# Kernel optimization log

Hardware: AMD Instinct MI355X
Metric: run time of the kernel (lower is better)

## Reference

```python
import jax, jax.numpy as jnp
import numpy as np
from jax import lax

EPS = 1e-5
NBIT = 127.0  # 8-bit symmetric: 2^(8-1)-1

def ste_round(x):
    return x + lax.stop_gradient(jnp.round(x) - x)

def quant_act(x, rng_max):
    # symmetric fake-quant of activations with learned per-cluster range
    s = rng_max / NBIT
    xq = jnp.clip(ste_round(x / s), -NBIT, NBIT) * s
    return xq, s

def fold_bn(w, gamma, beta, mean, var):
    std = jnp.sqrt(var + EPS)
    scale = gamma / std
    w_f = w * scale[:, None, None, None]
    b_f = beta - mean * scale
    return w_f, b_f

def quant_weight(w):
    # per-output-channel symmetric quant
    s = jnp.max(jnp.abs(w), axis=(1, 2, 3), keepdims=True) / NBIT
    wq = jnp.clip(ste_round(w / s), -NBIT, NBIT) * s
    return wq, s.reshape(-1)

def conv(x, w, stride=1, groups=1, pad=0):
    return lax.conv_general_dilated(
        x, w, window_strides=(stride, stride),
        padding=((pad, pad), (pad, pad)),
        dimension_numbers=('NCHW', 'OIHW', 'NCHW'),
        feature_group_count=groups)

def setup_inputs() -> dict:
    key = jax.random.key(0)
    ks = jax.random.split(key, 24)
    B, Cin, H, W = 64, 96, 28, 28
    Cmid, Cout, NC = 576, 96, 4
    d = {}
    d['x'] = jax.random.normal(ks[0], (B, Cin, H, W), dtype=jnp.float32)
    # conv1: 1x1 expansion
    d['w1'] = jax.random.normal(ks[1], (Cmid, Cin, 1, 1), jnp.float32) * 0.1
    d['g1'] = jax.random.uniform(ks[2], (Cmid,), minval=0.5, maxval=1.5)
    d['b1'] = jax.random.normal(ks[3], (Cmid,)) * 0.1
    d['m1'] = jax.random.normal(ks[4], (Cmid,)) * 0.1
    d['v1'] = jax.random.uniform(ks[5], (Cmid,), minval=0.5, maxval=1.5)
    # conv2: 3x3 depthwise
    d['w2'] = jax.random.normal(ks[6], (Cmid, 1, 3, 3), jnp.float32) * 0.1
    d['g2'] = jax.random.uniform(ks[7], (Cmid,), minval=0.5, maxval=1.5)
    d['b2'] = jax.random.normal(ks[8], (Cmid,)) * 0.1
    d['m2'] = jax.random.normal(ks[9], (Cmid,)) * 0.1
    d['v2'] = jax.random.uniform(ks[10], (Cmid,), minval=0.5, maxval=1.5)
    # conv3: 1x1 projection
    d['w3'] = jax.random.normal(ks[11], (Cout, Cmid, 1, 1), jnp.float32) * 0.1
    d['g3'] = jax.random.uniform(ks[12], (Cout,), minval=0.5, maxval=1.5)
    d['b3'] = jax.random.normal(ks[13], (Cout,)) * 0.1
    d['m3'] = jax.random.normal(ks[14], (Cout,)) * 0.1
    d['v3'] = jax.random.uniform(ks[15], (Cout,), minval=0.5, maxval=1.5)
    # per-cluster learned activation ranges for the 4 QuantAct modules
    d['r0'] = jax.random.uniform(ks[16], (NC,), minval=2.0, maxval=8.0)
    d['r1'] = jax.random.uniform(ks[17], (NC,), minval=2.0, maxval=8.0)
    d['r2'] = jax.random.uniform(ks[18], (NC,), minval=2.0, maxval=8.0)
    d['r3'] = jax.random.uniform(ks[19], (NC,), minval=2.0, maxval=8.0)
    d['cluster'] = 2
    return d

def reference(x, w1, g1, b1, m1, v1, w2, g2, b2, m2, v2,
              w3, g3, b3, m3, v3, r0, r1, r2, r3, cluster):
    identity = x  # residual path (in==out, stride==1)
    # QuantAct -> conv1 (BN-folded, per-channel quant) -> ReLU6
    xq, s0 = quant_act(x, r0[cluster])
    w1f, bf1 = fold_bn(w1, g1, b1, m1, v1)
    w1q, ws1 = quant_weight(w1f)
    y = conv(xq, w1q) + bf1[None, :, None, None]
    y = jnp.clip(y, 0.0, 6.0)
    # QuantAct1 -> depthwise conv2 -> ReLU6
    yq, s1 = quant_act(y, r1[cluster])
    w2f, bf2 = fold_bn(w2, g2, b2, m2, v2)
    w2q, ws2 = quant_weight(w2f)
    y = conv(yq, w2q, stride=1, groups=w2.shape[0], pad=1) + bf2[None, :, None, None]
    y = jnp.clip(y, 0.0, 6.0)
    # QuantAct2 -> conv3 projection
    yq, s2 = quant_act(y, r2[cluster])
    w3f, bf3 = fold_bn(w3, g3, b3, m3, v3)
    w3q, ws3 = quant_weight(w3f)
    y = conv(yq, w3q) + bf3[None, :, None, None]
    # residual add, then int32 requant
    y = y + identity
    out, s3 = quant_act(y, r3[cluster])
    return out, s3
```

## Files before the change

kernel.cpp:

```cpp
#include <hip/hip_runtime.h>
#include <cstdint>
#include <cstddef>

typedef int   v4i __attribute__((ext_vector_type(4)));
typedef float v4f __attribute__((ext_vector_type(4)));
typedef unsigned int u32;

constexpr int B_   = 64;
constexpr int CIN  = 96;
constexpr int P_   = 784;
constexpr int CMID = 576;
constexpr int COUT = 96;
constexpr int NOUT = B_ * COUT * P_;
constexpr float NBITF = 127.0f;
constexpr float EPSF  = 1e-5f;
constexpr float MAGICF = 12582912.0f;
constexpr int   BIASI  = 0x4B400000;

constexpr int Y1S = 43;

__device__ __forceinline__ int dot3(u32 a, u32 w, int acc) {
#if __has_builtin(__builtin_amdgcn_sdot4)
    return __builtin_amdgcn_sdot4((int)a, (int)w, acc, false);
#else
    return acc + (int)(signed char)(a)        * (int)(signed char)(w)
               + (int)(signed char)(a >> 8)   * (int)(signed char)(w >> 8)
               + (int)(signed char)(a >> 16)  * (int)(signed char)(w >> 16);
#endif
}

__device__ __forceinline__ void tr4(u32 S0, u32 S1, u32 S2, u32 S3, u32 O[4]) {
    u32 u01 = __builtin_amdgcn_perm(S1, S0, 0x05010400u);
    u32 u23 = __builtin_amdgcn_perm(S3, S2, 0x05010400u);
    u32 v01 = __builtin_amdgcn_perm(S1, S0, 0x07030602u);
    u32 v23 = __builtin_amdgcn_perm(S3, S2, 0x07030602u);
    O[0] = __builtin_amdgcn_perm(u23, u01, 0x05040100u);
    O[1] = __builtin_amdgcn_perm(u23, u01, 0x07060302u);
    O[2] = __builtin_amdgcn_perm(v23, v01, 0x05040100u);
    O[3] = __builtin_amdgcn_perm(v23, v01, 0x07060302u);
}

__device__ __forceinline__ u32 pack4(u32 t0, u32 t1, u32 t2, u32 t3) {
    u32 p01 = __builtin_amdgcn_perm(t1, t0, 0x05010400u);
    u32 p23 = __builtin_amdgcn_perm(t3, t2, 0x05010400u);
    return __builtin_amdgcn_perm(p23, p01, 0x05040100u);
}

__global__ __launch_bounds__(256)
void prep_w(const float* __restrict__ w1, const float* __restrict__ g1,
            const float* __restrict__ b1, const float* __restrict__ m1,
            const float* __restrict__ v1,
            const float* __restrict__ w2, const float* __restrict__ g2,
            const float* __restrict__ b2, const float* __restrict__ m2,
            const float* __restrict__ v2,
            const float* __restrict__ w3, const float* __restrict__ g3,
            const float* __restrict__ b3, const float* __restrict__ m3,
            const float* __restrict__ v3,
            const float* __restrict__ r0, const float* __restrict__ r1,
            const float* __restrict__ r2, const int* __restrict__ cluster,
            int8_t* __restrict__ w1qp, float2* __restrict__ e1,
            v4i* __restrict__ w2pk,    float2* __restrict__ e2,
            int8_t* __restrict__ w3qp, float2* __restrict__ e3)
{
    int tid = threadIdx.x;
    int c = cluster[0];
    int lane = tid & 63, wv = tid >> 6;
    int blk = blockIdx.x * 4 + wv;

    const float *w, *g, *bb, *mm, *vv;
    int oc, K, which;
    if (blk < CMID)            { which = 0; w = w1; g = g1; bb = b1; mm = m1; vv = v1; oc = blk;            K = CIN;  }
    else if (blk < 2 * CMID)   { which = 1; w = w2; g = g2; bb = b2; mm = m2; vv = v2; oc = blk - CMID;     K = 9;    }
    else                       { which = 2; w = w3; g = g3; bb = b3; mm = m3; vv = v3; oc = blk - 2 * CMID; K = CMID; }

    float scale = g[oc] / sqrtf(vv[oc] + EPSF);

    float mx = 0.f;
    for (int k = lane; k < K; k += 64)
        mx = fmaxf(mx, fabsf(w[oc * K + k] * scale));
    #pragma unroll
    for (int off = 1; off < 64; off <<= 1)
        mx = fmaxf(mx, __shfl_xor(mx, off));

    float s = mx / NBITF;

    int myq = 0;
    for (int k = lane; k < K; k += 64) {
        float wf = w[oc * K + k] * scale;
        float q  = fminf(fmaxf(rintf(wf / s), -127.f), 127.f);
        if (which == 0)      w1qp[oc * 144 + k] = (int8_t)q;
        else if (which == 1) myq = (int)q;
        else                 w3qp[oc * 592 + k] = (int8_t)q;
    }
    if (which == 0 && lane < 12)
        ((u32*)(w1qp + oc * 144))[24 + lane] = 0u;
    if (which == 1) {
        u32 qq[9];
        #pragma unroll
        for (int t = 0; t < 9; t++) qq[t] = (u32)__shfl(myq, t, 64) & 0xffu;
        if (lane == 0) {
            v4i pk;
            pk[0] = (int)(qq[0] | (qq[1] << 8) | (qq[2] << 16));
            pk[1] = (int)(qq[3] | (qq[4] << 8) | (qq[5] << 16));
            pk[2] = (int)(qq[6] | (qq[7] << 8) | (qq[8] << 16));
            pk[3] = 0;
            w2pk[oc] = pk;
        }
    }
    if (lane == 0) {
        float bf = bb[oc] - mm[oc] * scale;
        float s0 = r0[c] / NBITF, s1 = r1[c] / NBITF, s2 = r2[c] / NBITF;
        if (which == 0) {
            float inv_s1 = NBITF / r1[c];
            e1[oc] = make_float2(s0 * s * inv_s1, bf * inv_s1);
        } else if (which == 1) {
            float inv_s2 = NBITF / r2[c];
            e2[oc] = make_float2(s1 * s * inv_s2, bf * inv_s2);
        } else {
            e3[oc] = make_float2(s2 * s, bf);
        }
    }
}

__global__ __launch_bounds__(256, 2)
void conv123d(const v4i* __restrict__ w1q4,
              const float2* __restrict__ e1,
              const v4i* __restrict__ w2pk, const float2* __restrict__ e2,
              const int8_t* __restrict__ w3qp, const float2* __restrict__ e3,
              const float* __restrict__ x,
              const float* __restrict__ r0,
              const float* __restrict__ r1, const float* __restrict__ r2,
              const float* __restrict__ r3, const int* __restrict__ cluster,
              float* __restrict__ out)
{
    __shared__ v4i xw[11 * 8 * 16];
    __shared__ u32 y1s[4][48 * Y1S];
    __shared__ v4i y2c[12 * 112];

    int tid = threadIdx.x, b = blockIdx.y, rt = blockIdx.x;
    int R0 = 4 * rt;
    int W0 = (R0 - 1) * 28;
    int lane = tid & 63, wv = tid >> 6;
    int n = lane & 15, q4 = lane >> 4;

    int   c      = cluster[0];
    float inv_s0 = NBITF / r0[c];
    int   u1i    = (int)fminf(rintf(6.f * NBITF / r1[c]), 127.f);
    int   u2i    = (int)fminf(rintf(6.f * NBITF / r2[c]), 127.f);
    float s3     = r3[c] / NBITF;
    float inv_s3 = NBITF / r3[c];

    for (int i = tid; i < 4224; i += 256) {
        int nn = i & 15;
        int q  = (i >> 4) & 3;
        int gj = i >> 6;
        int g  = gj % 6, jm = gj / 6;
        int px = min(max(W0 + 16 * jm + nn, 0), P_ - 1);
        const float* xp = x + ((size_t)b * CIN + 16 * g + 4 * q) * P_ + px;
        int qv[4];
        #pragma unroll
        for (int j = 0; j < 4; j++) {
            float xf = xp[j * P_];
            qv[j] = (int)fminf(fmaxf(rintf(xf * inv_s0), -127.f), 127.f);
        }
        u32 t0 = __builtin_amdgcn_perm((u32)qv[1], (u32)qv[0], 0x00000400u);
        u32 t1 = __builtin_amdgcn_perm((u32)qv[3], (u32)qv[2], 0x00000400u);
        ((u32*)xw)[((jm * 8 + g) * 16 + nn) * 4 + q] =
            __builtin_amdgcn_perm(t1, t0, 0x05040100u);
    }
    for (int i = tid; i < 11 * 2 * 16; i += 256) {
        int nn = i & 15, gg = (i >> 4) & 1, jm = i >> 5;
        xw[(jm * 8 + 6 + gg) * 16 + nn] = (v4i){0, 0, 0, 0};
    }

    u32* myY1 = y1s[wv];

    int pxl0 = wv * 32 + n;
    int pxc0 = min(pxl0, 111);
    int pxc1 = min(pxl0 + 16, 111);
    const v4i* w34 = (const v4i*)w3qp;
    v4i acc3[2][6];
    #pragma unroll
    for (int h = 0; h < 2; h++)
        #pragma unroll
        for (int i = 0; i < 6; i++) acc3[h][i] = (v4i){0, 0, 0, 0};

    __syncthreads();

    for (int ph = 0; ph < 3; ph++) {
        int oc0 = ph * 192 + wv * 48;

        v4i    bw[3][2];
        float2 ee[3];
        #pragma unroll
        for (int jn = 0; jn < 3; jn++) {
            int oc = oc0 + 16 * jn + n;
            bw[jn][0] = w1q4[oc * 9 + q4];
            bw[jn][1] = w1q4[oc * 9 + 4 + q4];
            ee[jn] = e1[oc];
        }
        #pragma unroll
        for (int jm = 0; jm < 11; jm++) {
            v4i af0 = xw[(jm * 8 + q4) * 16 + n];
            v4i af1 = xw[(jm * 8 + 4 + q4) * 16 + n];
            int dw = 4 * jm + q4;
            bool inimg = (unsigned)(W0 + 4 * dw) < (unsigned)P_;

            #pragma unroll
            for (int jn = 0; jn < 3; jn++) {
                v4i acc = (v4i){0, 0, 0, 0};
                acc = __builtin_amdgcn_mfma_i32_16x16x64_i8(af0, bw[jn][0], acc, 0, 0, 0);
                acc = __builtin_amdgcn_mfma_i32_16x16x64_i8(af1, bw[jn][1], acc, 0, 0, 0);
                u32 t[4];
                #pragma unroll
                for (int r = 0; r < 4; r++) {
                    float f = fmaf((float)acc[r], ee[jn].x, ee[jn].y) + MAGICF;
                    t[r] = (u32)min(max(__float_as_int(f), BIASI), BIASI + u1i);
                }
                u32 pk = pack4(t[0], t[1], t[2], t[3]);
                if (dw < 42)
                    myY1[(16 * jn + n) * Y1S + dw] = inimg ? pk : 0u;
            }
        }

        #pragma unroll
        for (int p = 0; p < 3; p++) {
            int id   = p * 64 + lane;
            int chl  = id >> 2;
            int orow = id & 3;
            int ch   = oc0 + chl;
            int rb   = chl * Y1S + orow * 7;

            v4i wpk = w2pk[ch];
            u32 pk0 = (u32)wpk[0], pk1 = (u32)wpk[1], pk2 = (u32)wpk[2];
            float2 e = e2[ch];

            u32 W[3][7];
            #pragma unroll
            for (int r = 0; r < 3; r++)
                #pragma unroll
                for (int w = 0; w < 7; w++)
                    W[r][w] = myY1[rb + r * 7 + w];

            __builtin_amdgcn_sched_barrier(0);

            u32 outw[7];
            #pragma unroll
            for (int xq = 0; xq < 7; xq++) {
                u32 M0 = xq ? W[0][xq - 1] : 0u;
                u32 M1 = xq ? W[1][xq - 1] : 0u;
                u32 M2 = xq ? W[2][xq - 1] : 0u;
                u32 D0 = W[0][xq], D1 = W[1][xq], D2 = W[2][xq];
                u32 N0 = (xq < 6) ? W[0][xq + 1] : 0u;
                u32 N1 = (xq < 6) ? W[1][xq + 1] : 0u;
                u32 N2 = (xq < 6) ? W[2][xq + 1] : 0u;

                int a0, a1, a2, a3;
                a0 = dot3(__builtin_amdgcn_alignbyte(D0, M0, 3), pk0, 0);
                a0 = dot3(__builtin_amdgcn_alignbyte(D1, M1, 3), pk1, a0);
                a0 = dot3(__builtin_amdgcn_alignbyte(D2, M2, 3), pk2, a0);
                a1 = dot3(D0, pk0, 0);
                a1 = dot3(D1, pk1, a1);
                a1 = dot3(D2, pk2, a1);
                a2 = dot3(__builtin_amdgcn_alignbyte(N0, D0, 1), pk0, 0);
                a2 = dot3(__builtin_amdgcn_alignbyte(N1, D1, 1), pk1, a2);
                a2 = dot3(__builtin_amdgcn_alignbyte(N2, D2, 1), pk2, a2);
                a3 = dot3(__builtin_amdgcn_alignbyte(N0, D0, 2), pk0, 0);
                a3 = dot3(__builtin_amdgcn_alignbyte(N1, D1, 2), pk1, a3);
                a3 = dot3(__builtin_amdgcn_alignbyte(N2, D2, 2), pk2, a3);

                int aa[4] = {a0, a1, a2, a3};
                u32 tq[4];
                #pragma unroll
                for (int i = 0; i < 4; i++) {
                    float f = fmaf((float)aa[i], e.x, e.y) + MAGICF;
                    tq[i] = (u32)min(max(__float_as_int(f), BIASI), BIASI + u2i);
                }
                outw[xq] = pack4(tq[0], tq[1], tq[2], tq[3]);
            }

            #pragma unroll
            for (int xq = 0; xq < 7; xq++)
                myY1[chl * Y1S + orow * 7 + xq] = outw[xq];
        }

        for (int u = lane; u < 84; u += 64) {
            int kgl = u / 28, d = u - kgl * 28;
            u32 O[4][4];
            #pragma unroll
            for (int j = 0; j < 4; j++) {
                int ch0 = 16 * kgl + 4 * j;
                tr4(myY1[(ch0 + 0) * Y1S + d], myY1[(ch0 + 1) * Y1S + d],
                    myY1[(ch0 + 2) * Y1S + d], myY1[(ch0 + 3) * Y1S + d], O[j]);
            }
            int kgG = wv * 3 + kgl;
            #pragma unroll
            for (int i = 0; i < 4; i++)
                y2c[kgG * 112 + 4 * d + i] =
                    (v4i){(int)O[0][i], (int)O[1][i], (int)O[2][i], (int)O[3][i]};
        }

        __syncthreads();

        #pragma unroll
        for (int ks = 0; ks < 3; ks++) {
            v4i bfr0 = y2c[(4 * ks + q4) * 112 + pxc0];
            v4i bfr1 = y2c[(4 * ks + q4) * 112 + pxc1];
            #pragma unroll
            for (int i = 0; i < 6; i++) {
                v4i afr = w34[(i * 16 + n) * 37 + ph * 12 + 4 * ks + q4];
                acc3[0][i] = __builtin_amdgcn_mfma_i32_16x16x64_i8(afr, bfr0, acc3[0][i], 0, 0, 0);
                acc3[1][i] = __builtin_amdgcn_mfma_i32_16x16x64_i8(afr, bfr1, acc3[1][i], 0, 0, 0);
            }
        }

        if (ph < 2) __syncthreads();
    }

    #pragma unroll
    for (int h = 0; h < 2; h++) {
        int pxl = pxl0 + 16 * h;
        if (pxl < 112) {
            int px = R0 * 28 + pxl;
            #pragma unroll
            for (int i = 0; i < 6; i++) {
                #pragma unroll
                for (int r = 0; r < 4; r++) {
                    int    oc = i * 16 + q4 * 4 + r;
                    float2 e  = e3[oc];
                    size_t gi = (size_t)(b * COUT + oc) * P_ + px;
                    float v  = fmaf((float)acc3[h][i][r], e.x, e.y) + x[gi];
                    float f  = fmaf(v, inv_s3, MAGICF);
                    int lvl  = min(max(__float_as_int(f) - BIASI, -127), 127);
                    out[gi]  = (float)lvl * s3;
                }
            }
        }
    }
    if (rt == 0 && b == 0 && tid == 0)
        out[NOUT] = s3;
}

extern "C" void kernel_launch(void* const* d_in, const int* in_sizes, int n_in,
                              void* d_out, int out_size, void* d_ws, size_t ws_size,
                              hipStream_t stream)
{
    const float* x  = (const float*)d_in[0];
    const float* w1 = (const float*)d_in[1];
    const float* g1 = (const float*)d_in[2];
    const float* b1 = (const float*)d_in[3];
    const float* m1 = (const float*)d_in[4];
    const float* v1 = (const float*)d_in[5];
    const float* w2 = (const float*)d_in[6];
    const float* g2 = (const float*)d_in[7];
    const float* b2 = (const float*)d_in[8];
    const float* m2 = (const float*)d_in[9];
    const float* v2 = (const float*)d_in[10];
    const float* w3 = (const float*)d_in[11];
    const float* g3 = (const float*)d_in[12];
    const float* b3 = (const float*)d_in[13];
    const float* m3 = (const float*)d_in[14];
    const float* v3 = (const float*)d_in[15];
    const float* r0 = (const float*)d_in[16];
    const float* r1 = (const float*)d_in[17];
    const float* r2 = (const float*)d_in[18];
    const float* r3 = (const float*)d_in[19];
    const int*   cl = (const int*)d_in[20];

    float* out = (float*)d_out;

    char*  ws  = (char*)d_ws;
    size_t off = 0;
    auto carve = [&](size_t bytes) {
        size_t cur = off;
        off = (off + bytes + 255) & ~(size_t)255;
        return (void*)(ws + cur);
    };
    int8_t* w1qp = (int8_t*)carve((size_t)CMID * 144);
    float2* e1   = (float2*)carve((size_t)CMID * 8);
    v4i*    w2pk = (v4i*)carve((size_t)CMID * 16);
    float2* e2   = (float2*)carve((size_t)CMID * 8);
    int8_t* w3qp = (int8_t*)carve((size_t)COUT * 592);
    float2* e3   = (float2*)carve((size_t)COUT * 8);
    (void)ws_size; (void)in_sizes; (void)n_in; (void)out_size;

    prep_w<<<dim3(312), dim3(256), 0, stream>>>(
        w1, g1, b1, m1, v1, w2, g2, b2, m2, v2, w3, g3, b3, m3, v3,
        r0, r1, r2, cl,
        w1qp, e1, w2pk, e2, w3qp, e3);

    conv123d<<<dim3(7, B_), dim3(256), 0, stream>>>(
        (const v4i*)w1qp, e1, w2pk, e2, w3qp, e3,
        x, r0, r1, r2, r3, cl, out);
}
```

Measured before the change: 156.6 us.

## Pre-quantize input to int8 MFMA layout in prep kernel, read directly from global

Input quantization and transposition into the int8 MFMA fragment layout move out of the fused conv kernel into extra blocks of the prep kernel, which write a global int8 buffer. The conv kernel then loads A fragments straight from global memory instead of staging them through LDS. This drops the xw shared array and the initial barrier, shrinks the Y1 stride, and raises launch bounds to allow 3 blocks per CU. In exchange it adds a global round trip for the quantized input and a serial dependency on the larger prep launch, and the fragment loads inside the MFMA loop now have global-memory latency.

```diff
diff --git a/kernel.cpp b/kernel.cpp
--- a/kernel.cpp
+++ b/kernel.cpp
@@ -17,7 +17,8 @@
 constexpr float MAGICF = 12582912.0f;
 constexpr int   BIASI  = 0x4B400000;
 
-constexpr int Y1S = 43;
+constexpr int XB4 = 13 * 8 * 64;
+constexpr int Y1S = 42;
 
 __device__ __forceinline__ int dot3(u32 a, u32 w, int acc) {
 #if __has_builtin(__builtin_amdgcn_sdot4)
@@ -47,25 +48,66 @@
 }
 
 __global__ __launch_bounds__(256)
-void prep_w(const float* __restrict__ w1, const float* __restrict__ g1,
-            const float* __restrict__ b1, const float* __restrict__ m1,
-            const float* __restrict__ v1,
-            const float* __restrict__ w2, const float* __restrict__ g2,
-            const float* __restrict__ b2, const float* __restrict__ m2,
-            const float* __restrict__ v2,
-            const float* __restrict__ w3, const float* __restrict__ g3,
-            const float* __restrict__ b3, const float* __restrict__ m3,
-            const float* __restrict__ v3,
-            const float* __restrict__ r0, const float* __restrict__ r1,
-            const float* __restrict__ r2, const int* __restrict__ cluster,
-            int8_t* __restrict__ w1qp, float2* __restrict__ e1,
-            v4i* __restrict__ w2pk,    float2* __restrict__ e2,
-            int8_t* __restrict__ w3qp, float2* __restrict__ e3)
+void prep_all(const float* __restrict__ x,
+              const float* __restrict__ w1, const float* __restrict__ g1,
+              const float* __restrict__ b1, const float* __restrict__ m1,
+              const float* __restrict__ v1,
+              const float* __restrict__ w2, const float* __restrict__ g2,
+              const float* __restrict__ b2, const float* __restrict__ m2,
+              const float* __restrict__ v2,
+              const float* __restrict__ w3, const float* __restrict__ g3,
+              const float* __restrict__ b3, const float* __restrict__ m3,
+              const float* __restrict__ v3,
+              const float* __restrict__ r0, const float* __restrict__ r1,
+              const float* __restrict__ r2, const int* __restrict__ cluster,
+              u32* __restrict__ x8t2,
+              int8_t* __restrict__ w1qp, float2* __restrict__ e1,
+              v4i* __restrict__ w2pk,    float2* __restrict__ e2,
+              int8_t* __restrict__ w3qp, float2* __restrict__ e3)
 {
+    __shared__ u32 T[112 * 37];
     int tid = threadIdx.x;
     int c = cluster[0];
+
+    if (blockIdx.x < 448) {
+        int pt0 = blockIdx.x % 7, b = blockIdx.x / 7;
+        float inv_s0 = NBITF / r0[c];
+
+        for (int i = tid; i < 112 * 8; i += 256) {
+            int row = i >> 3, cc = 24 + (i & 7);
+            T[row * 37 + cc] = 0u;
+        }
+        for (int u = tid; u < 24 * 28; u += 256) {
+            int pq = u % 28, icq = u / 28;
+            int pxb = pt0 * 112 + pq * 4;
+            int q[4][4];
+            #pragma unroll
+            for (int j = 0; j < 4; j++) {
+                v4f xv = *(const v4f*)(x + ((size_t)b * CIN + icq * 4 + j) * P_ + pxb);
+                #pragma unroll
+                for (int i = 0; i < 4; i++)
+                    q[j][i] = (int)fminf(fmaxf(rintf(xv[i] * inv_s0), -127.f), 127.f);
+            }
+            #pragma unroll
+            for (int i = 0; i < 4; i++) {
+                u32 t0 = __builtin_amdgcn_perm((u32)q[1][i], (u32)q[0][i], 0x00000400u);
+                u32 t1 = __builtin_amdgcn_perm((u32)q[3][i], (u32)q[2][i], 0x00000400u);
+                T[(pq * 4 + i) * 37 + icq] = __builtin_amdgcn_perm(t1, t0, 0x05040100u);
+            }
+        }
+        __syncthreads();
+        u32* gb = x8t2 + (size_t)b * XB4 * 4;
+        for (int i = tid; i < 32 * 112; i += 256) {
+            int icq = i / 112, pxo = i - icq * 112;
+            int px = pt0 * 112 + pxo;
+            gb[(((px >> 6) * 8 + (icq >> 2)) * 64 + (px & 63)) * 4 + (icq & 3)] =
+                T[pxo * 37 + icq];
+        }
+        return;
+    }
+
     int lane = tid & 63, wv = tid >> 6;
-    int blk = blockIdx.x * 4 + wv;
+    int blk = (blockIdx.x - 448) * 4 + wv;
 
     const float *w, *g, *bb, *mm, *vv;
     int oc, K, which;
@@ -122,18 +164,16 @@
     }
 }
 
-__global__ __launch_bounds__(256, 2)
-void conv123d(const v4i* __restrict__ w1q4,
+__global__ __launch_bounds__(256, 3)
+void conv123d(const v4i* __restrict__ x8t2, const v4i* __restrict__ w1q4,
               const float2* __restrict__ e1,
               const v4i* __restrict__ w2pk, const float2* __restrict__ e2,
               const int8_t* __restrict__ w3qp, const float2* __restrict__ e3,
               const float* __restrict__ x,
-              const float* __restrict__ r0,
               const float* __restrict__ r1, const float* __restrict__ r2,
               const float* __restrict__ r3, const int* __restrict__ cluster,
               float* __restrict__ out)
 {
-    __shared__ v4i xw[11 * 8 * 16];
     __shared__ u32 y1s[4][48 * Y1S];
     __shared__ v4i y2c[12 * 112];
 
@@ -144,33 +184,17 @@
     int n = lane & 15, q4 = lane >> 4;
 
     int   c      = cluster[0];
-    float inv_s0 = NBITF / r0[c];
     int   u1i    = (int)fminf(rintf(6.f * NBITF / r1[c]), 127.f);
     int   u2i    = (int)fminf(rintf(6.f * NBITF / r2[c]), 127.f);
     float s3     = r3[c] / NBITF;
     float inv_s3 = NBITF / r3[c];
 
-    for (int i = tid; i < 4224; i += 256) {
-        int nn = i & 15;
-        int q  = (i >> 4) & 3;
-        int gj = i >> 6;
-        int g  = gj % 6, jm = gj / 6;
-        int px = min(max(W0 + 16 * jm + nn, 0), P_ - 1);
-        const float* xp = x + ((size_t)b * CIN + 16 * g + 4 * q) * P_ + px;
-        int qv[4];
-        #pragma unroll
-        for (int j = 0; j < 4; j++) {
-            float xf = xp[j * P_];
-            qv[j] = (int)fminf(fmaxf(rintf(xf * inv_s0), -127.f), 127.f);
-        }
-        u32 t0 = __builtin_amdgcn_perm((u32)qv[1], (u32)qv[0], 0x00000400u);
-        u32 t1 = __builtin_amdgcn_perm((u32)qv[3], (u32)qv[2], 0x00000400u);
-        ((u32*)xw)[((jm * 8 + g) * 16 + nn) * 4 + q] =
-            __builtin_amdgcn_perm(t1, t0, 0x05040100u);
-    }
-    for (int i = tid; i < 11 * 2 * 16; i += 256) {
-        int nn = i & 15, gg = (i >> 4) & 1, jm = i >> 5;
-        xw[(jm * 8 + 6 + gg) * 16 + nn] = (v4i){0, 0, 0, 0};
+    const v4i* xb = x8t2 + (size_t)b * XB4;
+    int pb[11];
+    #pragma unroll
+    for (int jm = 0; jm < 11; jm++) {
+        int px = min(max(W0 + 16 * jm + n, 0), P_ - 1);
+        pb[jm] = (px >> 6) * 512 + (px & 63);
     }
 
     u32* myY1 = y1s[wv];
@@ -185,8 +209,6 @@
         #pragma unroll
         for (int i = 0; i < 6; i++) acc3[h][i] = (v4i){0, 0, 0, 0};
 
-    __syncthreads();
-
     for (int ph = 0; ph < 3; ph++) {
         int oc0 = ph * 192 + wv * 48;
 
@@ -201,8 +223,8 @@
         }
         #pragma unroll
         for (int jm = 0; jm < 11; jm++) {
-            v4i af0 = xw[(jm * 8 + q4) * 16 + n];
-            v4i af1 = xw[(jm * 8 + 4 + q4) * 16 + n];
+            v4i af0 = xb[pb[jm] + q4 * 64];
+            v4i af1 = xb[pb[jm] + (4 + q4) * 64];
             int dw = 4 * jm + q4;
             bool inimg = (unsigned)(W0 + 4 * dw) < (unsigned)P_;
 
@@ -382,14 +404,15 @@
     float2* e2   = (float2*)carve((size_t)CMID * 8);
     int8_t* w3qp = (int8_t*)carve((size_t)COUT * 592);
     float2* e3   = (float2*)carve((size_t)COUT * 8);
+    u32*    x8t2 = (u32*)carve((size_t)B_ * XB4 * 16);
     (void)ws_size; (void)in_sizes; (void)n_in; (void)out_size;
 
-    prep_w<<<dim3(312), dim3(256), 0, stream>>>(
-        w1, g1, b1, m1, v1, w2, g2, b2, m2, v2, w3, g3, b3, m3, v3,
-        r0, r1, r2, cl,
+    prep_all<<<dim3(760), dim3(256), 0, stream>>>(
+        x, w1, g1, b1, m1, v1, w2, g2, b2, m2, v2, w3, g3, b3, m3, v3,
+        r0, r1, r2, cl, x8t2,
         w1qp, e1, w2pk, e2, w3qp, e3);
 
     conv123d<<<dim3(7, B_), dim3(256), 0, stream>>>(
-        (const v4i*)w1qp, e1, w2pk, e2, w3qp, e3,
-        x, r0, r1, r2, r3, cl, out);
-}
+        (const v4i*)x8t2, (const v4i*)w1qp, e1, w2pk, e2, w3qp, e3,
+        x, r1, r2, r3, cl, out);
+}
```

After: 168.4 us. 7.5% more time.
